# Kernel tuning notes

Measured on AMD Instinct MI355X. Metric: run time of the kernel, lower is better.

## Reference

```python
import math
import jax, jax.numpy as jnp
import numpy as np

EMBED_DIM = 1024
NUM_HEADS = 16
HEAD_DIM = EMBED_DIM // NUM_HEADS


def setup_inputs() -> dict:
    key = jax.random.key(0)
    ks = jax.random.split(key, 10)
    B, S, E = 2, 2048, EMBED_DIM
    x = jax.random.normal(ks[0], (B, S, E), dtype=jnp.float32)
    mask = jax.random.randint(ks[1], (B, S), 0, 2, dtype=jnp.int32)
    s = 1.0 / math.sqrt(E)
    Wq = jax.random.normal(ks[2], (E, E), dtype=jnp.float32) * s
    bq = jnp.zeros((E,), dtype=jnp.float32)
    Wk = jax.random.normal(ks[3], (E, E), dtype=jnp.float32) * s
    bk = jnp.zeros((E,), dtype=jnp.float32)
    Wv = jax.random.normal(ks[4], (E, E), dtype=jnp.float32) * s
    bv = jnp.zeros((E,), dtype=jnp.float32)
    Wo = jax.random.normal(ks[5], (E, E), dtype=jnp.float32) * s
    bo = jnp.zeros((E,), dtype=jnp.float32)
    return {"x": x, "mask": mask, "Wq": Wq, "bq": bq, "Wk": Wk, "bk": bk,
            "Wv": Wv, "bv": bv, "Wo": Wo, "bo": bo}


def reference(x, mask, Wq, bq, Wk, bk, Wv, bv, Wo, bo):
    B, S, E = x.shape
    H, D = NUM_HEADS, HEAD_DIM
    scale = math.sqrt(D)  # ScaledDotProductAttention built with head_dim

    def split_heads(t):
        return t.reshape(B, S, H, D).transpose(0, 2, 1, 3)  # [B,H,S,D]

    q = split_heads(x @ Wq + bq)
    k = split_heads(x @ Wk + bk)
    v = split_heads(x @ Wv + bv)

    scores = jnp.einsum('bhqd,bhkd->bhqk', q, k) / scale  # [B,H,S,S]
    m = mask[:, None, None, :].astype(scores.dtype)        # [B,1,1,S]
    neg = jnp.finfo(scores.dtype).min
    scores = jnp.where(m == 0, neg, scores)
    aw = jax.nn.softmax(scores, axis=-1)
    # post-softmax mask renormalization (as in the torch module)
    aw = aw * m
    denom = aw.sum(axis=-1, keepdims=True)
    aw = jnp.where(denom > 0, aw / jnp.where(denom > 0, denom, 1.0), 0.0)

    ctx = jnp.einsum('bhqk,bhkd->bhqd', aw, v)             # [B,H,S,D]
    ctx = ctx.transpose(0, 2, 1, 3).reshape(B, S, E)
    out = ctx @ Wo + bo
    return out
```

## Files before the change

kernel.cpp:

```cpp
#include <hip/hip_runtime.h>

typedef _Float16 half8 __attribute__((ext_vector_type(8)));
typedef _Float16 half4v __attribute__((ext_vector_type(4)));
typedef _Float16 h2 __attribute__((ext_vector_type(2)));
typedef float f4 __attribute__((ext_vector_type(4)));

#define ASYNC_COPY16(ldsp, gp)                                                     \
  __builtin_amdgcn_global_load_lds((__attribute__((address_space(1))) void*)(gp),  \
                                   (__attribute__((address_space(3))) void*)(ldsp),\
                                   16, 0, 0)

__device__ __forceinline__ f4 mfma16(half8 a, half8 b, f4 c) {
  return __builtin_amdgcn_mfma_f32_16x16x32_f16(a, b, c, 0, 0, 0);
}

__device__ __forceinline__ h2 pack2(float a, float b) {
  return __builtin_bit_cast(h2, __builtin_amdgcn_cvt_pkrtz(a, b));
}

#if defined(__has_builtin)
#if __has_builtin(__builtin_amdgcn_exp2f)
#define EXP2(x) __builtin_amdgcn_exp2f(x)
#endif
#if __has_builtin(__builtin_amdgcn_fdot2)
#define FDOT2(a, b, c) __builtin_amdgcn_fdot2((a), (b), (c), false)
#endif
#endif
#ifndef EXP2
#define EXP2(x) __expf((x) * 0.69314718056f)
#endif
#define KSCALE 0.18033688011f
#define FIXMAX 10.0f


__global__ __launch_bounds__(256) void k_cvt_x(const float* __restrict__ x,
                                               _Float16* __restrict__ xh) {
  int i = (blockIdx.x * 256 + threadIdx.x) * 4;
  f4 v = *(const f4*)(x + i);
  half4v h;
  h[0] = (_Float16)v[0]; h[1] = (_Float16)v[1];
  h[2] = (_Float16)v[2]; h[3] = (_Float16)v[3];
  *(half4v*)(xh + i) = h;
}

__global__ __launch_bounds__(256) void k_transpose_w(
    const float* __restrict__ Wq, const float* __restrict__ Wk,
    const float* __restrict__ Wv, const float* __restrict__ Wo,
    _Float16* __restrict__ wqkvT, _Float16* __restrict__ woT) {
  __shared__ float tw[32][33];
  int z = blockIdx.z;
  const float* w = (z == 0) ? Wq : (z == 1) ? Wk : (z == 2) ? Wv : Wo;
  _Float16* wt = (z == 3) ? woT : wqkvT + (size_t)z * 1048576;
  int k0 = blockIdx.y * 32, n0 = blockIdx.x * 32;
  int tx = threadIdx.x, ty = threadIdx.y;
  for (int j = 0; j < 32; j += 8) tw[ty + j][tx] = w[(size_t)(k0 + ty + j) * 1024 + n0 + tx];
  __syncthreads();
  for (int j = 0; j < 32; j += 8)
    wt[(size_t)(n0 + ty + j) * 1024 + k0 + tx] = (_Float16)tw[tx][ty + j];
}

__global__ __launch_bounds__(256) void k_gemm_proj(
    const _Float16* __restrict__ A, const _Float16* __restrict__ Bt,
    const float* __restrict__ bq, const float* __restrict__ bk, const float* __restrict__ bv,
    _Float16* __restrict__ Qo, _Float16* __restrict__ Ko, _Float16* __restrict__ Vto) {
  __shared__ __align__(16) _Float16 As[128 * 32];
  __shared__ __align__(16) _Float16 Bs[128 * 32];
  const int t = threadIdx.x, lane = t & 63, w = t >> 6;
  const int qd = lane >> 4, lr = lane & 15;
  const int m0 = blockIdx.y * 128, n0 = blockIdx.x * 128;
  const int wm = (w & 1) * 64, wn = (w >> 1) * 64;
  const f4 z4 = {0.f, 0.f, 0.f, 0.f};
  f4 acc[4][4];
#pragma unroll
  for (int i = 0; i < 4; ++i)
#pragma unroll
    for (int j = 0; j < 4; ++j) acc[i][j] = z4;

  const int c0 = t, c1 = t + 256;
  for (int k0 = 0; k0 < 1024; k0 += 32) {
    const _Float16* ga0 = A + (size_t)(m0 + (c0 >> 2)) * 1024 + k0 + (c0 & 3) * 8;
    const _Float16* ga1 = A + (size_t)(m0 + (c1 >> 2)) * 1024 + k0 + (c1 & 3) * 8;
    const _Float16* gb0 = Bt + (size_t)(n0 + (c0 >> 2)) * 1024 + k0 + (c0 & 3) * 8;
    const _Float16* gb1 = Bt + (size_t)(n0 + (c1 >> 2)) * 1024 + k0 + (c1 & 3) * 8;
    char* la = (char*)As + w * 1024;
    char* lb = (char*)Bs + w * 1024;
    ASYNC_COPY16(la, ga0);
    ASYNC_COPY16(la + 4096, ga1);
    ASYNC_COPY16(lb, gb0);
    ASYNC_COPY16(lb + 4096, gb1);
    __syncthreads();
    half8 af[4], bf[4];
#pragma unroll
    for (int i = 0; i < 4; ++i)
      af[i] = *(const half8*)(As + (wm + i * 16 + lr) * 32 + qd * 8);
#pragma unroll
    for (int j = 0; j < 4; ++j)
      bf[j] = *(const half8*)(Bs + (wn + j * 16 + lr) * 32 + qd * 8);
#pragma unroll
    for (int i = 0; i < 4; ++i)
#pragma unroll
      for (int j = 0; j < 4; ++j) acc[i][j] = mfma16(af[i], bf[j], acc[i][j]);
    __syncthreads();
  }

  const int mat = n0 >> 10;
  const float* bias = (mat == 0) ? bq : (mat == 1) ? bk : bv;
  if (mat == 2) {
#pragma unroll
    for (int i = 0; i < 4; ++i)
#pragma unroll
      for (int j = 0; j < 4; ++j) {
        int n = (n0 + wn + j * 16 + lr) & 1023;
        int hh = n >> 6, d = n & 63;
        int mb = m0 + wm + i * 16 + qd * 4;
        int bb = mb >> 11, sb = mb & 2047;
        float bval = bias[n];
        half4v hv;
#pragma unroll
        for (int r = 0; r < 4; ++r) hv[r] = (_Float16)(acc[i][j][r] + bval);
        *(half4v*)(Vto + ((size_t)(bb * 16 + hh) * 64 + d) * 2048 + sb) = hv;
      }
  } else {
    _Float16* outp = (mat == 0) ? Qo : Ko;
    const float scl = (mat == 0) ? KSCALE : 1.f;
#pragma unroll
    for (int i = 0; i < 4; ++i)
#pragma unroll
      for (int j = 0; j < 4; ++j)
#pragma unroll
        for (int r = 0; r < 4; ++r) {
          int m = m0 + wm + i * 16 + qd * 4 + r;
          int n = (n0 + wn + j * 16 + lr) & 1023;
          float v = (acc[i][j][r] + bias[n]) * scl;
          int bb = m >> 11, s = m & 2047, hh = n >> 6, d = n & 63;
          outp[(size_t)((bb * 16 + hh) * 2048 + s) * 64 + d] = (_Float16)v;
        }
  }
}

__global__ __launch_bounds__(256, 2) void k_attn(
    const _Float16* __restrict__ Qg, const _Float16* __restrict__ Kg,
    const _Float16* __restrict__ Vtg, const int* __restrict__ maskg,
    _Float16* __restrict__ Op, float* __restrict__ ml) {
  __shared__ __align__(16) _Float16 Ks[64][72];
  __shared__ __align__(16) _Float16 Vts[64][72];
  __shared__ __align__(16) _Float16 Pq[4][16][72];
  __shared__ float Msk[64];

  const int bh = blockIdx.y;
  const int b = bh >> 4;
  const int q0 = blockIdx.x * 128;
  const int z = blockIdx.z;
  const int kb = z * 1024;
  const int t = threadIdx.x, lane = t & 63, w = t >> 6;
  const int qd = lane >> 4, lr = lane & 15;

  half8 qf[2][2];
#pragma unroll
  for (int rt = 0; rt < 2; ++rt)
#pragma unroll
    for (int ks = 0; ks < 2; ++ks)
      qf[rt][ks] = *(const half8*)(Qg + (size_t)(bh * 2048 + q0 + w * 32 + rt * 16 + lr) * 64 +
                                   ks * 32 + qd * 8);

  float l_i[2] = {0.f, 0.f};
  const f4 z4 = {0.f, 0.f, 0.f, 0.f};
  f4 O[2][4];
#pragma unroll
  for (int rt = 0; rt < 2; ++rt)
#pragma unroll
    for (int dt = 0; dt < 4; ++dt) O[rt][dt] = z4;

  const int sr0 = t >> 3, scc = (t & 7) * 8;
  const int sr1 = sr0 + 32;
  const _Float16* Kbase = Kg + (size_t)bh * 2048 * 64 + (size_t)kb * 64;
  const _Float16* Vtbase = Vtg + (size_t)bh * 64 * 2048 + kb;

  f4 kr0 = *(const f4*)(Kbase + (size_t)sr0 * 64 + scc);
  f4 kr1 = *(const f4*)(Kbase + (size_t)sr1 * 64 + scc);
  f4 vr0 = *(const f4*)(Vtbase + (size_t)sr0 * 2048 + scc);
  f4 vr1 = *(const f4*)(Vtbase + (size_t)sr1 * 2048 + scc);
  float mval = 0.f;
  if (t < 64) mval = maskg[b * 2048 + kb + t] ? -FIXMAX : -30010.f;

#if defined(FDOT2)
  const h2 one2 = {(_Float16)1.f, (_Float16)1.f};
#endif

  for (int it = 0; it < 16; ++it) {
    __syncthreads();
    *(f4*)&Ks[sr0][scc] = kr0;
    *(f4*)&Ks[sr1][scc] = kr1;
    *(f4*)&Vts[sr0][scc] = vr0;
    *(f4*)&Vts[sr1][scc] = vr1;
    if (t < 64) Msk[t] = mval;
    __syncthreads();

    if (it < 15) {
      int kk = (it + 1) * 64;
      kr0 = *(const f4*)(Kbase + (size_t)(kk + sr0) * 64 + scc);
      kr1 = *(const f4*)(Kbase + (size_t)(kk + sr1) * 64 + scc);
      vr0 = *(const f4*)(Vtbase + (size_t)sr0 * 2048 + kk + scc);
      vr1 = *(const f4*)(Vtbase + (size_t)sr1 * 2048 + kk + scc);
      if (t < 64) mval = maskg[b * 2048 + kb + kk + t] ? -FIXMAX : -30010.f;
    }

    f4 sc[2][4];
#pragma unroll
    for (int kt = 0; kt < 4; ++kt) {
      f4 mv = *(const f4*)&Msk[kt * 16 + qd * 4];
      sc[0][kt] = mv;
      sc[1][kt] = mv;
    }
#pragma unroll
    for (int kt = 0; kt < 4; ++kt) {
      half8 k0 = *(const half8*)&Ks[kt * 16 + lr][qd * 8];
      half8 k1 = *(const half8*)&Ks[kt * 16 + lr][32 + qd * 8];
      sc[0][kt] = mfma16(k0, qf[0][0], sc[0][kt]);
      sc[0][kt] = mfma16(k1, qf[0][1], sc[0][kt]);
      sc[1][kt] = mfma16(k0, qf[1][0], sc[1][kt]);
      sc[1][kt] = mfma16(k1, qf[1][1], sc[1][kt]);
    }

#pragma unroll
    for (int rt = 0; rt < 2; ++rt) {
      float s = 0.f;
#pragma unroll
      for (int kt = 0; kt < 4; ++kt) {
        float p0 = EXP2(sc[rt][kt][0]);
        float p1 = EXP2(sc[rt][kt][1]);
        float p2 = EXP2(sc[rt][kt][2]);
        float p3 = EXP2(sc[rt][kt][3]);
        h2 pa = pack2(p0, p1);
        h2 pb = pack2(p2, p3);
#if defined(FDOT2)
        s = FDOT2(pa, one2, s);
        s = FDOT2(pb, one2, s);
#else
        s += p0 + p1 + p2 + p3;
#endif
        half4v hv;
        hv.lo = pa;
        hv.hi = pb;
        *(half4v*)&Pq[w][lr][kt * 16 + qd * 4] = hv;
      }
      s += __shfl_xor(s, 16, 64);
      s += __shfl_xor(s, 32, 64);
      l_i[rt] += s;

      half8 bp0 = *(const half8*)&Pq[w][lr][qd * 8];
      half8 bp1 = *(const half8*)&Pq[w][lr][32 + qd * 8];
#pragma unroll
      for (int dt = 0; dt < 4; ++dt) {
        half8 va0 = *(const half8*)&Vts[dt * 16 + lr][qd * 8];
        half8 va1 = *(const half8*)&Vts[dt * 16 + lr][32 + qd * 8];
        O[rt][dt] = mfma16(va0, bp0, O[rt][dt]);
        O[rt][dt] = mfma16(va1, bp1, O[rt][dt]);
      }
    }
  }

#pragma unroll
  for (int rt = 0; rt < 2; ++rt) {
    int qrow = q0 + w * 32 + rt * 16 + lr;
    size_t rowi = (size_t)(z * 32 + bh) * 2048 + qrow;
    _Float16* op = Op + rowi * 64;
#pragma unroll
    for (int dt = 0; dt < 4; ++dt) {
      half4v hv;
#pragma unroll
      for (int r = 0; r < 4; ++r) hv[r] = (_Float16)O[rt][dt][r];
      *(half4v*)(op + dt * 16 + qd * 4) = hv;
    }
    if (qd == 0) ml[rowi] = l_i[rt];
  }
}

__global__ __launch_bounds__(256) void k_merge(const _Float16* __restrict__ Op,
                                               const float* __restrict__ ml,
                                               _Float16* __restrict__ ctx) {
  int idx = blockIdx.x * 256 + threadIdx.x;
  int d8 = (idx & 7) * 8;
  int h = (idx >> 3) & 15;
  int q = idx >> 7;
  int b = q >> 11, s = q & 2047;
  int bh = b * 16 + h;
  size_t r1 = (size_t)bh * 2048 + s;
  size_t r2 = (size_t)(32 + bh) * 2048 + s;
  float l1 = ml[r1], l2 = ml[r2];
  float inv = 1.f / fmaxf(l1 + l2, 1e-20f);
  half8 o1 = *(const half8*)(Op + r1 * 64 + d8);
  half8 o2 = *(const half8*)(Op + r2 * 64 + d8);
  half8 ho;
#pragma unroll
  for (int j = 0; j < 8; ++j)
    ho[j] = (_Float16)(((float)o1[j] + (float)o2[j]) * inv);
  *(half8*)(ctx + (size_t)q * 1024 + h * 64 + d8) = ho;
}

__global__ __launch_bounds__(256) void k_gemm_out(
    const _Float16* __restrict__ A, const _Float16* __restrict__ Bt,
    const float* __restrict__ bo, float* __restrict__ out) {
  __shared__ __align__(16) _Float16 As[64 * 32];
  __shared__ __align__(16) _Float16 Bs[128 * 32];
  const int t = threadIdx.x, lane = t & 63, w = t >> 6;
  const int qd = lane >> 4, lr = lane & 15;
  const int m0 = blockIdx.y * 64, n0 = blockIdx.x * 128;
  const int wm = (w & 1) * 32, wn = (w >> 1) * 64;
  const f4 z4 = {0.f, 0.f, 0.f, 0.f};
  f4 acc[2][4];
#pragma unroll
  for (int i = 0; i < 2; ++i)
#pragma unroll
    for (int j = 0; j < 4; ++j) acc[i][j] = z4;

  const int c0 = t, c1 = t + 256;
  for (int k0 = 0; k0 < 1024; k0 += 32) {
    const _Float16* ga = A + (size_t)(m0 + (t >> 2)) * 1024 + k0 + (t & 3) * 8;
    const _Float16* gb0 = Bt + (size_t)(n0 + (c0 >> 2)) * 1024 + k0 + (c0 & 3) * 8;
    const _Float16* gb1 = Bt + (size_t)(n0 + (c1 >> 2)) * 1024 + k0 + (c1 & 3) * 8;
    char* la = (char*)As + w * 1024;
    char* lb = (char*)Bs + w * 1024;
    ASYNC_COPY16(la, ga);
    ASYNC_COPY16(lb, gb0);
    ASYNC_COPY16(lb + 4096, gb1);
    __syncthreads();
    half8 af[2], bf[4];
#pragma unroll
    for (int i = 0; i < 2; ++i)
      af[i] = *(const half8*)(As + (wm + i * 16 + lr) * 32 + qd * 8);
#pragma unroll
    for (int j = 0; j < 4; ++j)
      bf[j] = *(const half8*)(Bs + (wn + j * 16 + lr) * 32 + qd * 8);
#pragma unroll
    for (int i = 0; i < 2; ++i)
#pragma unroll
      for (int j = 0; j < 4; ++j) acc[i][j] = mfma16(af[i], bf[j], acc[i][j]);
    __syncthreads();
  }
#pragma unroll
  for (int i = 0; i < 2; ++i)
#pragma unroll
    for (int j = 0; j < 4; ++j)
#pragma unroll
      for (int r = 0; r < 4; ++r) {
        int m = m0 + wm + i * 16 + qd * 4 + r;
        int n = n0 + wn + j * 16 + lr;
        out[(size_t)m * 1024 + n] = acc[i][j][r] + bo[n];
      }
}

extern "C" void kernel_launch(void* const* d_in, const int* in_sizes, int n_in,
                              void* d_out, int out_size, void* d_ws, size_t ws_size,
                              hipStream_t stream) {
  const float* x = (const float*)d_in[0];
  const int* mask = (const int*)d_in[1];
  const float* Wq = (const float*)d_in[2];
  const float* bq = (const float*)d_in[3];
  const float* Wk = (const float*)d_in[4];
  const float* bk = (const float*)d_in[5];
  const float* Wv = (const float*)d_in[6];
  const float* bv = (const float*)d_in[7];
  const float* Wo = (const float*)d_in[8];
  const float* bo = (const float*)d_in[9];
  float* out = (float*)d_out;
  char* ws = (char*)d_ws;
  const size_t MB = 1 << 20;

  _Float16* Oph   = (_Float16*)(ws + 0);
  _Float16* xh    = (_Float16*)(ws + 0);
  _Float16* wqkvT = (_Float16*)(ws + 8 * MB);
  _Float16* woT   = (_Float16*)(ws + 16 * MB);
  _Float16* Qh    = (_Float16*)(ws + 18 * MB);
  _Float16* ctxh  = (_Float16*)(ws + 18 * MB);
  _Float16* Kh    = (_Float16*)(ws + 26 * MB);
  _Float16* Vth   = (_Float16*)(ws + 34 * MB);
  float*    mlw   = (float*)   (ws + 42 * MB);

  k_cvt_x<<<dim3(4096), dim3(256), 0, stream>>>(x, xh);
  k_transpose_w<<<dim3(32, 32, 4), dim3(32, 8), 0, stream>>>(Wq, Wk, Wv, Wo, wqkvT, woT);
  k_gemm_proj<<<dim3(24, 32), dim3(256), 0, stream>>>(xh, wqkvT, bq, bk, bv, Qh, Kh, Vth);
  k_attn<<<dim3(16, 32, 2), dim3(256), 0, stream>>>(Qh, Kh, Vth, mask, Oph, mlw);
  k_merge<<<dim3(2048), dim3(256), 0, stream>>>(Oph, mlw, ctxh);
  k_gemm_out<<<dim3(8, 64), dim3(256), 0, stream>>>(ctxh, woT, bo, out);
}
```

Measured before the change: 205.8 us.

## Fuse prep kernels, merge split-K attention into out GEMM, deepen proj K-tile

Combines the x conversion and weight transpose into one launch. Folds the split-attention merge and normalization into the output GEMM's A-tile load, which removes the ctx round trip through memory and one kernel launch. Doubles the projection GEMM K-step to 64 so there are half as many barriers per block. The costs are larger LDS use in the projection GEMM and synchronous global loads in the output GEMM, where the A tile previously came in through async copies.

```diff
diff --git a/kernel.cpp b/kernel.cpp
--- a/kernel.cpp
+++ b/kernel.cpp
@@ -33,26 +33,28 @@
 #define FIXMAX 10.0f
 
 
-__global__ __launch_bounds__(256) void k_cvt_x(const float* __restrict__ x,
-                                               _Float16* __restrict__ xh) {
-  int i = (blockIdx.x * 256 + threadIdx.x) * 4;
-  f4 v = *(const f4*)(x + i);
-  half4v h;
-  h[0] = (_Float16)v[0]; h[1] = (_Float16)v[1];
-  h[2] = (_Float16)v[2]; h[3] = (_Float16)v[3];
-  *(half4v*)(xh + i) = h;
-}
-
-__global__ __launch_bounds__(256) void k_transpose_w(
+__global__ __launch_bounds__(256) void k_prep(
+    const float* __restrict__ x, _Float16* __restrict__ xh,
     const float* __restrict__ Wq, const float* __restrict__ Wk,
     const float* __restrict__ Wv, const float* __restrict__ Wo,
     _Float16* __restrict__ wqkvT, _Float16* __restrict__ woT) {
   __shared__ float tw[32][33];
-  int z = blockIdx.z;
+  const int bid = blockIdx.x, t = threadIdx.x;
+  if (bid < 4096) {
+    int i = (bid * 256 + t) * 4;
+    f4 v = *(const f4*)(x + i);
+    half4v h;
+    h[0] = (_Float16)v[0]; h[1] = (_Float16)v[1];
+    h[2] = (_Float16)v[2]; h[3] = (_Float16)v[3];
+    *(half4v*)(xh + i) = h;
+    return;
+  }
+  const int idx = bid - 4096;
+  const int z = idx >> 10, rem = idx & 1023;
+  const int n0 = (rem & 31) * 32, k0 = (rem >> 5) * 32;
   const float* w = (z == 0) ? Wq : (z == 1) ? Wk : (z == 2) ? Wv : Wo;
   _Float16* wt = (z == 3) ? woT : wqkvT + (size_t)z * 1048576;
-  int k0 = blockIdx.y * 32, n0 = blockIdx.x * 32;
-  int tx = threadIdx.x, ty = threadIdx.y;
+  const int tx = t & 31, ty = t >> 5;
   for (int j = 0; j < 32; j += 8) tw[ty + j][tx] = w[(size_t)(k0 + ty + j) * 1024 + n0 + tx];
   __syncthreads();
   for (int j = 0; j < 32; j += 8)
@@ -63,8 +65,8 @@
     const _Float16* __restrict__ A, const _Float16* __restrict__ Bt,
     const float* __restrict__ bq, const float* __restrict__ bk, const float* __restrict__ bv,
     _Float16* __restrict__ Qo, _Float16* __restrict__ Ko, _Float16* __restrict__ Vto) {
-  __shared__ __align__(16) _Float16 As[128 * 32];
-  __shared__ __align__(16) _Float16 Bs[128 * 32];
+  __shared__ __align__(16) _Float16 As[128 * 64];
+  __shared__ __align__(16) _Float16 Bs[128 * 64];
   const int t = threadIdx.x, lane = t & 63, w = t >> 6;
   const int qd = lane >> 4, lr = lane & 15;
   const int m0 = blockIdx.y * 128, n0 = blockIdx.x * 128;
@@ -76,30 +78,33 @@
 #pragma unroll
     for (int j = 0; j < 4; ++j) acc[i][j] = z4;
 
-  const int c0 = t, c1 = t + 256;
-  for (int k0 = 0; k0 < 1024; k0 += 32) {
-    const _Float16* ga0 = A + (size_t)(m0 + (c0 >> 2)) * 1024 + k0 + (c0 & 3) * 8;
-    const _Float16* ga1 = A + (size_t)(m0 + (c1 >> 2)) * 1024 + k0 + (c1 & 3) * 8;
-    const _Float16* gb0 = Bt + (size_t)(n0 + (c0 >> 2)) * 1024 + k0 + (c0 & 3) * 8;
-    const _Float16* gb1 = Bt + (size_t)(n0 + (c1 >> 2)) * 1024 + k0 + (c1 & 3) * 8;
-    char* la = (char*)As + w * 1024;
-    char* lb = (char*)Bs + w * 1024;
-    ASYNC_COPY16(la, ga0);
-    ASYNC_COPY16(la + 4096, ga1);
-    ASYNC_COPY16(lb, gb0);
-    ASYNC_COPY16(lb + 4096, gb1);
-    __syncthreads();
-    half8 af[4], bf[4];
-#pragma unroll
-    for (int i = 0; i < 4; ++i)
-      af[i] = *(const half8*)(As + (wm + i * 16 + lr) * 32 + qd * 8);
-#pragma unroll
-    for (int j = 0; j < 4; ++j)
-      bf[j] = *(const half8*)(Bs + (wn + j * 16 + lr) * 32 + qd * 8);
-#pragma unroll
-    for (int i = 0; i < 4; ++i)
-#pragma unroll
-      for (int j = 0; j < 4; ++j) acc[i][j] = mfma16(af[i], bf[j], acc[i][j]);
+  for (int k0 = 0; k0 < 1024; k0 += 64) {
+#pragma unroll
+    for (int j = 0; j < 4; ++j) {
+      int c = t + j * 256;
+      int row = c >> 3, col = (c & 7) * 8;
+      const _Float16* ga = A + (size_t)(m0 + row) * 1024 + k0 + col;
+      const _Float16* gb = Bt + (size_t)(n0 + row) * 1024 + k0 + col;
+      char* la = (char*)As + j * 4096 + w * 1024;
+      char* lb = (char*)Bs + j * 4096 + w * 1024;
+      ASYNC_COPY16(la, ga);
+      ASYNC_COPY16(lb, gb);
+    }
+    __syncthreads();
+#pragma unroll
+    for (int ks = 0; ks < 2; ++ks) {
+      half8 af[4], bf[4];
+#pragma unroll
+      for (int i = 0; i < 4; ++i)
+        af[i] = *(const half8*)(As + (wm + i * 16 + lr) * 64 + ks * 32 + qd * 8);
+#pragma unroll
+      for (int j = 0; j < 4; ++j)
+        bf[j] = *(const half8*)(Bs + (wn + j * 16 + lr) * 64 + ks * 32 + qd * 8);
+#pragma unroll
+      for (int i = 0; i < 4; ++i)
+#pragma unroll
+        for (int j = 0; j < 4; ++j) acc[i][j] = mfma16(af[i], bf[j], acc[i][j]);
+    }
     __syncthreads();
   }
 
@@ -276,31 +281,10 @@
   }
 }
 
-__global__ __launch_bounds__(256) void k_merge(const _Float16* __restrict__ Op,
-                                               const float* __restrict__ ml,
-                                               _Float16* __restrict__ ctx) {
-  int idx = blockIdx.x * 256 + threadIdx.x;
-  int d8 = (idx & 7) * 8;
-  int h = (idx >> 3) & 15;
-  int q = idx >> 7;
-  int b = q >> 11, s = q & 2047;
-  int bh = b * 16 + h;
-  size_t r1 = (size_t)bh * 2048 + s;
-  size_t r2 = (size_t)(32 + bh) * 2048 + s;
-  float l1 = ml[r1], l2 = ml[r2];
-  float inv = 1.f / fmaxf(l1 + l2, 1e-20f);
-  half8 o1 = *(const half8*)(Op + r1 * 64 + d8);
-  half8 o2 = *(const half8*)(Op + r2 * 64 + d8);
-  half8 ho;
-#pragma unroll
-  for (int j = 0; j < 8; ++j)
-    ho[j] = (_Float16)(((float)o1[j] + (float)o2[j]) * inv);
-  *(half8*)(ctx + (size_t)q * 1024 + h * 64 + d8) = ho;
-}
-
 __global__ __launch_bounds__(256) void k_gemm_out(
-    const _Float16* __restrict__ A, const _Float16* __restrict__ Bt,
-    const float* __restrict__ bo, float* __restrict__ out) {
+    const _Float16* __restrict__ Op, const float* __restrict__ ml,
+    const _Float16* __restrict__ Bt, const float* __restrict__ bo,
+    float* __restrict__ out) {
   __shared__ __align__(16) _Float16 As[64 * 32];
   __shared__ __align__(16) _Float16 Bs[128 * 32];
   const int t = threadIdx.x, lane = t & 63, w = t >> 6;
@@ -314,16 +298,27 @@
 #pragma unroll
     for (int j = 0; j < 4; ++j) acc[i][j] = z4;
 
+  const int arow = t >> 2, acol = (t & 3) * 8;
+  const int m = m0 + arow, b = m >> 11, s = m & 2047;
   const int c0 = t, c1 = t + 256;
   for (int k0 = 0; k0 < 1024; k0 += 32) {
-    const _Float16* ga = A + (size_t)(m0 + (t >> 2)) * 1024 + k0 + (t & 3) * 8;
+    int e = k0 + acol;
+    int h = e >> 6, d = e & 63;
+    size_t r1 = (size_t)(b * 16 + h) * 2048 + s;
+    size_t r2 = r1 + 32 * 2048;
+    half8 o1 = *(const half8*)(Op + r1 * 64 + d);
+    half8 o2 = *(const half8*)(Op + r2 * 64 + d);
+    float L = ml[r1] + ml[r2];
+    _Float16 hinv = (_Float16)(1.f / fmaxf(L, 1e-20f));
     const _Float16* gb0 = Bt + (size_t)(n0 + (c0 >> 2)) * 1024 + k0 + (c0 & 3) * 8;
     const _Float16* gb1 = Bt + (size_t)(n0 + (c1 >> 2)) * 1024 + k0 + (c1 & 3) * 8;
-    char* la = (char*)As + w * 1024;
     char* lb = (char*)Bs + w * 1024;
-    ASYNC_COPY16(la, ga);
     ASYNC_COPY16(lb, gb0);
     ASYNC_COPY16(lb + 4096, gb1);
+    half8 a;
+#pragma unroll
+    for (int j = 0; j < 8; ++j) a[j] = (_Float16)((o1[j] + o2[j]) * hinv);
+    *(half8*)(As + arow * 32 + acol) = a;
     __syncthreads();
     half8 af[2], bf[4];
 #pragma unroll
@@ -344,9 +339,9 @@
     for (int j = 0; j < 4; ++j)
 #pragma unroll
       for (int r = 0; r < 4; ++r) {
-        int m = m0 + wm + i * 16 + qd * 4 + r;
+        int mm = m0 + wm + i * 16 + qd * 4 + r;
         int n = n0 + wn + j * 16 + lr;
-        out[(size_t)m * 1024 + n] = acc[i][j][r] + bo[n];
+        out[(size_t)mm * 1024 + n] = acc[i][j][r] + bo[n];
       }
 }
 
@@ -372,15 +367,12 @@
   _Float16* wqkvT = (_Float16*)(ws + 8 * MB);
   _Float16* woT   = (_Float16*)(ws + 16 * MB);
   _Float16* Qh    = (_Float16*)(ws + 18 * MB);
-  _Float16* ctxh  = (_Float16*)(ws + 18 * MB);
   _Float16* Kh    = (_Float16*)(ws + 26 * MB);
   _Float16* Vth   = (_Float16*)(ws + 34 * MB);
   float*    mlw   = (float*)   (ws + 42 * MB);
 
-  k_cvt_x<<<dim3(4096), dim3(256), 0, stream>>>(x, xh);
-  k_transpose_w<<<dim3(32, 32, 4), dim3(32, 8), 0, stream>>>(Wq, Wk, Wv, Wo, wqkvT, woT);
+  k_prep<<<dim3(8192), dim3(256), 0, stream>>>(x, xh, Wq, Wk, Wv, Wo, wqkvT, woT);
   k_gemm_proj<<<dim3(24, 32), dim3(256), 0, stream>>>(xh, wqkvT, bq, bk, bv, Qh, Kh, Vth);
   k_attn<<<dim3(16, 32, 2), dim3(256), 0, stream>>>(Qh, Kh, Vth, mask, Oph, mlw);
-  k_merge<<<dim3(2048), dim3(256), 0, stream>>>(Oph, mlw, ctxh);
-  k_gemm_out<<<dim3(8, 64), dim3(256), 0, stream>>>(ctxh, woT, bo, out);
-}
+  k_gemm_out<<<dim3(8, 64), dim3(256), 0, stream>>>(Oph, mlw, woT, bo, out);
+}
```

Result: slower. 223.5 us (+8.6%).
